# Kernel optimization log

Hardware: AMD Instinct MI355X
Metric: run time of the kernel (lower is better)

## Reference

```python
import jax, jax.numpy as jnp
import numpy as np

GN_GROUPS = 32
GN_EPS = 1e-5


def conv3x3(x, w, b=None):
    # x: [B,C,H,W], w: [O,I,3,3]
    y = jax.lax.conv_general_dilated(x, w, (1, 1), 'SAME',
                                     dimension_numbers=('NCHW', 'OIHW', 'NCHW'))
    if b is not None:
        y = y + b[None, :, None, None]
    return y


def group_norm(x, gamma, beta):
    B, C, H, W = x.shape
    xg = x.reshape(B, GN_GROUPS, C // GN_GROUPS, H, W)
    mu = xg.mean(axis=(2, 3, 4), keepdims=True)
    var = ((xg - mu) ** 2).mean(axis=(2, 3, 4), keepdims=True)
    xn = ((xg - mu) * jax.lax.rsqrt(var + GN_EPS)).reshape(B, C, H, W)
    return xn * gamma[None, :, None, None] + beta[None, :, None, None]


def tower(x, ws, gammas, betas):
    # ws: [n_conv, C, C, 3, 3]; conv(bias=False) -> GroupNorm -> ReLU, n_conv times
    for i in range(ws.shape[0]):
        x = jax.nn.relu(group_norm(conv3x3(x, ws[i]), gammas[i], betas[i]))
    return x


def setup_inputs() -> dict:
    key = jax.random.key(0)
    ks = jax.random.split(key, 20)
    C, n_conv, n_fg = 256, 4, 20  # n_class - 1 = 20
    prior = 0.01
    B = 2
    sizes = [(100, 100), (50, 50), (25, 25), (13, 13), (7, 7)]
    inp = {}
    for i, (h, w) in enumerate(sizes):
        inp[f'feat{i}'] = jax.random.normal(ks[i], (B, C, h, w), dtype=jnp.float32)
    std = 0.01  # init_conv_std
    inp['cls_tw_w'] = std * jax.random.normal(ks[5], (n_conv, C, C, 3, 3), dtype=jnp.float32)
    inp['cls_tw_g'] = jnp.ones((n_conv, C), dtype=jnp.float32)
    inp['cls_tw_b'] = jnp.zeros((n_conv, C), dtype=jnp.float32)
    inp['box_tw_w'] = std * jax.random.normal(ks[6], (n_conv, C, C, 3, 3), dtype=jnp.float32)
    inp['box_tw_g'] = jnp.ones((n_conv, C), dtype=jnp.float32)
    inp['box_tw_b'] = jnp.zeros((n_conv, C), dtype=jnp.float32)
    inp['cls_pred_w'] = std * jax.random.normal(ks[7], (n_fg, C, 3, 3), dtype=jnp.float32)
    prior_bias = -np.log((1.0 - prior) / prior)
    inp['cls_pred_b'] = jnp.full((n_fg,), prior_bias, dtype=jnp.float32)
    inp['box_pred_w'] = std * jax.random.normal(ks[8], (4, C, 3, 3), dtype=jnp.float32)
    inp['box_pred_b'] = jnp.zeros((4,), dtype=jnp.float32)
    inp['ctr_pred_w'] = std * jax.random.normal(ks[9], (1, C, 3, 3), dtype=jnp.float32)
    inp['ctr_pred_b'] = jnp.zeros((1,), dtype=jnp.float32)
    inp['scales'] = jnp.ones((5,), dtype=jnp.float32)
    return inp


def reference(feat0, feat1, feat2, feat3, feat4,
              cls_tw_w, cls_tw_g, cls_tw_b,
              box_tw_w, box_tw_g, box_tw_b,
              cls_pred_w, cls_pred_b,
              box_pred_w, box_pred_b,
              ctr_pred_w, ctr_pred_b,
              scales):
    feats = [feat0, feat1, feat2, feat3, feat4]
    logits, bboxes, centers = [], [], []
    for i, feat in enumerate(feats):
        c = tower(feat, cls_tw_w, cls_tw_g, cls_tw_b)
        logits.append(conv3x3(c, cls_pred_w, cls_pred_b))
        centers.append(conv3x3(c, ctr_pred_w, ctr_pred_b))
        b = tower(feat, box_tw_w, box_tw_g, box_tw_b)
        bboxes.append(jnp.exp(conv3x3(b, box_pred_w, box_pred_b) * scales[i]))
    return tuple(logits + bboxes + centers)
```

## Files before the change

kernel.cpp:

```cpp
#include <hip/hip_runtime.h>
#include <hip/hip_bf16.h>
#include <cstdint>

typedef unsigned short u16;
typedef __attribute__((ext_vector_type(8))) short short8;
typedef __attribute__((ext_vector_type(4))) float floatx4;
typedef __attribute__((ext_vector_type(4))) int intx4;

#define PA_TOTAL 13696
#define CCH 256
#define KTOT 2304

struct Tables {
  int H[5], W[5], P[5], base[5], tile0[5];
  int lb[5], bb[5], cb[5];
};
struct FeatPtrs { const float* f[5]; };
struct ConvArgs {
  const u16* X[2];
  const u16* Wt[2];
  u16* outB[2];
  float* stats;
  float* dout;
  const float* biasCls; const float* biasCtr; const float* biasBox; const float* scales;
};
struct ReorderArgs {
  const float* cls_w; const float* box_w; const float* pcls_w; const float* ctr_w; const float* pbox_w;
  u16* wrCls; u16* wrBox; u16* wrPCls; u16* wrPBox;
};

__device__ __forceinline__ u16 f2bf(float f) {
  union { float f; unsigned u; } v; v.f = f;
  unsigned r = v.u + 0x7fffu + ((v.u >> 16) & 1u);
  return (u16)(r >> 16);
}
__device__ __forceinline__ float bf2f(u16 h) {
  union { unsigned u; float f; } v; v.u = ((unsigned)h) << 16;
  return v.f;
}

__device__ __forceinline__ void gload16(const void* g, void* l) {
  __builtin_amdgcn_global_load_lds(
      (const __attribute__((address_space(1))) void*)g,
      (__attribute__((address_space(3))) void*)l, 16, 0, 0);
}

__global__ void reorder_all(ReorderArgs ra) {
  __shared__ float row[KTOT];
  const int r = blockIdx.x;
  const float* s;
  u16* o;
  if (r < 1024)      { s = ra.cls_w  + (size_t)r * KTOT;          o = ra.wrCls  + (size_t)r * KTOT; }
  else if (r < 2048) { int q = r - 1024; s = ra.box_w  + (size_t)q * KTOT; o = ra.wrBox  + (size_t)q * KTOT; }
  else if (r < 2068) { int q = r - 2048; s = ra.pcls_w + (size_t)q * KTOT; o = ra.wrPCls + (size_t)q * KTOT; }
  else if (r == 2068){ s = ra.ctr_w;                               o = ra.wrPCls + (size_t)20 * KTOT; }
  else if (r < 2073) { int q = r - 2069; s = ra.pbox_w + (size_t)q * KTOT; o = ra.wrPBox + (size_t)q * KTOT; }
  else if (r < 2084) {
    u16* oz = ra.wrPCls + (size_t)(21 + (r - 2073)) * KTOT;
#pragma unroll
    for (int j = 0; j < 9; ++j) oz[threadIdx.x + j * 256] = 0;
    return;
  } else {
    u16* oz = ra.wrPBox + (size_t)(4 + (r - 2084)) * KTOT;
#pragma unroll
    for (int j = 0; j < 9; ++j) oz[threadIdx.x + j * 256] = 0;
    return;
  }
#pragma unroll
  for (int j = 0; j < 9; ++j) row[threadIdx.x + j * 256] = s[threadIdx.x + j * 256];
  __syncthreads();
#pragma unroll
  for (int j = 0; j < 9; ++j) {
    int k = threadIdx.x + j * 256;
    o[k] = f2bf(row[(k & 255) * 9 + (k >> 8)]);
  }
}

__global__ void convert_inputs(FeatPtrs fp, u16* __restrict__ out, Tables tb) {
  __shared__ float tile[32][33];
  const int pt = blockIdx.x, c32 = blockIdx.y, b = blockIdx.z;
  const int p0 = pt * 32;
  int lvl = 0;
#pragma unroll
  for (int i = 1; i < 5; ++i) if (p0 >= tb.base[i]) lvl = i;
  const int P = tb.P[lvl];
  const int pl0 = p0 - tb.base[lvl];
  const int r = threadIdx.x >> 5, col = threadIdx.x & 31;
  const float* src = fp.f[lvl] + ((size_t)b * CCH + c32 * 32) * P;
#pragma unroll
  for (int i = 0; i < 4; ++i) {
    int crow = r + i * 8;
    int pl = pl0 + col;
    tile[crow][col] = (pl < P) ? src[(size_t)crow * P + pl] : 0.f;
  }
  __syncthreads();
#pragma unroll
  for (int i = 0; i < 4; ++i) {
    int px = r + i * 8;
    out[((size_t)b * PA_TOTAL + p0 + px) * CCH + c32 * 32 + col] = f2bf(tile[col][px]);
  }
}

__global__ __launch_bounds__(256) void conv_tower(ConvArgs a, Tables tb) {
  const int L = blockIdx.x + 107 * (blockIdx.y + 2 * blockIdx.z);
  const int xcd = L & 7, slot = L >> 3;
  const int tower = xcd >> 2, mt = (xcd >> 1) & 1, b = xcd & 1, t = slot;
  int lvl = 0;
#pragma unroll
  for (int i = 1; i < 5; ++i) if (t >= tb.tile0[i]) lvl = i;
  const int H = tb.H[lvl], W = tb.W[lvl], P = tb.P[lvl], base = tb.base[lvl];
  const int n0 = (t - tb.tile0[lvl]) * 128;

  const int tid = threadIdx.x;
  const int lane = tid & 63, wv = tid >> 6;
  const int wm = wv >> 1, wn = wv & 1;

  __shared__ u16 ldsAll[2 * 8192];

  const char* Xb = (const char*)(a.X[tower] + ((size_t)b * PA_TOTAL + base) * CCH);
  const char* Wb = (const char*)(a.Wt[tower] + (size_t)(mt * 128) * KTOT);

  const int qsw2 = (((lane & 3) ^ ((lane >> 2) & 3) ^ ((lane >> 4) & 3))) * 16;
  int xoffG[2];
  unsigned mask9[2];
  int xl[2];
#pragma unroll
  for (int k = 0; k < 2; ++k) {
    const int g = wv + 4 * k;
    const int prow = n0 + 16 * g + (lane >> 2);
    int rr = prow / W, cc = prow - rr * W;
    unsigned m = 0;
#pragma unroll
    for (int tap = 0; tap < 9; ++tap) {
      const int dh = tap / 3 - 1, dw = tap % 3 - 1;
      bool v = ((unsigned)(rr + dh) < (unsigned)H) & ((unsigned)(cc + dw) < (unsigned)W);
      m |= ((unsigned)v) << tap;
    }
    mask9[k] = m;
    xoffG[k] = prow * 512 + qsw2;
    xl[k] = g * 1024;
  }
  const int padbase = P * 512 + qsw2;
  int woffG[2];
#pragma unroll
  for (int k = 0; k < 2; ++k) {
    const int wrow = 16 * (wv + 4 * k) + (lane >> 2);
    woffG[k] = wrow * (KTOT * 2) + qsw2;
  }

  const int arow = lane & 15, kq = lane >> 4;
  const int csw0 = ((kq ^ (arow & 3) ^ ((arow >> 2) & 3))) * 16;
  int rbA[4], rbX[4];
#pragma unroll
  for (int i = 0; i < 4; ++i) {
    rbA[i] = (wm * 64 + i * 16 + arow) * 64 + csw0;
    rbX[i] = (wn * 64 + i * 16 + arow) * 64 + csw0;
  }

  floatx4 acc[4][4];
#pragma unroll
  for (int i = 0; i < 4; ++i)
#pragma unroll
    for (int j = 0; j < 4; ++j) acc[i][j] = (floatx4)0.f;

  {
    const int doff0 = (-W - 1) * 512;
#pragma unroll
    for (int k = 0; k < 2; ++k) {
      const int off = (mask9[k] & 1u) ? (xoffG[k] + doff0) : padbase;
      gload16(Xb + off, (char*)ldsAll + xl[k]);
    }
#pragma unroll
    for (int k = 0; k < 2; ++k)
      gload16(Wb + woffG[k], (char*)ldsAll + 8192 + xl[k]);
  }

  int pb = 0;
#pragma unroll 1
  for (int icb2 = 0; icb2 < 8; ++icb2) {
#pragma unroll
    for (int tap = 0; tap < 9; ++tap) {
      asm volatile("s_barrier" ::: "memory");
      if (!(icb2 == 7 && tap == 8)) {
        const int ntap = (tap == 8) ? 0 : tap + 1;
        const int nic  = (tap == 8) ? icb2 + 1 : icb2;
        const int ndh = ntap / 3;
        const int ndoff = ((ndh - 1) * W + (ntap - 3 * ndh - 1)) * 512;
        const int nslice = nic * 64;
        char* bufN = (char*)ldsAll + (pb ^ 1) * 16384;
#pragma unroll
        for (int k = 0; k < 2; ++k) {
          const int off = ((((mask9[k] >> ntap) & 1u) ? (xoffG[k] + ndoff) : padbase)) + nslice;
          gload16(Xb + off, bufN + xl[k]);
        }
        const int nko = ntap * 512 + nslice;
#pragma unroll
        for (int k = 0; k < 2; ++k)
          gload16(Wb + woffG[k] + nko, bufN + 8192 + xl[k]);
        asm volatile("s_waitcnt vmcnt(4)\n\ts_barrier" ::: "memory");
      } else {
        asm volatile("s_waitcnt vmcnt(0)\n\ts_barrier" ::: "memory");
      }
      const char* bufc = (const char*)ldsAll + pb * 16384;
      __builtin_amdgcn_s_setprio(1);
      short8 af[4], bv[4];
#pragma unroll
      for (int i = 0; i < 4; ++i) af[i] = *(const short8*)(bufc + 8192 + rbA[i]);
#pragma unroll
      for (int j = 0; j < 4; ++j) bv[j] = *(const short8*)(bufc + rbX[j]);
#pragma unroll
      for (int i = 0; i < 4; ++i)
#pragma unroll
        for (int j = 0; j < 4; ++j)
          acc[i][j] = __builtin_amdgcn_mfma_f32_16x16x32_bf16(af[i], bv[j], acc[i][j], 0, 0, 0);
      __builtin_amdgcn_s_setprio(0);
      pb ^= 1;
    }
  }

  const int quad = lane >> 4, col = lane & 15;
  u16* convB = a.outB[tower];
  float s[4] = {0.f, 0.f, 0.f, 0.f}, ss[4] = {0.f, 0.f, 0.f, 0.f};
#pragma unroll
  for (int j = 0; j < 4; ++j) {
    int pl = n0 + wn * 64 + j * 16 + col;
    bool valid = pl < P;
    u16* dst = convB + ((size_t)b * PA_TOTAL + base + pl) * CCH + mt * 128 + wm * 64 + quad * 4;
#pragma unroll
    for (int i = 0; i < 4; ++i) {
      ushort4 hv;
#pragma unroll
      for (int r = 0; r < 4; ++r) {
        u16 hh = f2bf(acc[i][j][r]);
        ((u16*)&hv)[r] = hh;
        float vr = bf2f(hh);
        if (valid) { s[i] += vr; ss[i] += vr * vr; }
      }
      if (valid) *(ushort4*)(dst + i * 16) = hv;
    }
  }
#pragma unroll
  for (int i = 0; i < 4; ++i) {
#pragma unroll
    for (int off = 16; off >= 1; off >>= 1) {
      s[i] += __shfl_down(s[i], off, 64);
      ss[i] += __shfl_down(ss[i], off, 64);
    }
  }
  if ((lane & 31) == 0) {
    int half = lane >> 5;
#pragma unroll
    for (int i = 0; i < 4; ++i) {
      float* st = a.stats + tower * 640 +
                  ((size_t)((b * 5 + lvl) * 32 + mt * 16 + wm * 8 + i * 2 + half)) * 2;
      atomicAdd(st, s[i]);
      atomicAdd(st + 1, ss[i]);
    }
  }
}

__global__ __launch_bounds__(256) void conv_pred(ConvArgs a, Tables tb) {
  constexpr int NI = 1;
  constexpr int WROWS = 32;
  const int L = blockIdx.x + 108 * (blockIdx.y + 2 * blockIdx.z);
  const int xcd = L & 7, slot = L >> 3;
  const int tower = xcd >> 2, b = (xcd >> 1) & 1;
  const int t = slot * 2 + (xcd & 1);
  if (t >= 107) return;
  int lvl = 0;
#pragma unroll
  for (int i = 1; i < 5; ++i) if (t >= tb.tile0[i]) lvl = i;
  const int H = tb.H[lvl], W = tb.W[lvl], P = tb.P[lvl], base = tb.base[lvl];
  const int n0 = (t - tb.tile0[lvl]) * 128;

  const int tid = threadIdx.x;
  const int lane = tid & 63, wv = tid >> 6;
  const int wm = wv >> 1, wn = wv & 1;

  __shared__ u16 ldsAll[128 * 64 + WROWS * 64];
  u16* ldsX = ldsAll;
  u16* ldsW = ldsAll + 128 * 64;

  const char* Xb = (const char*)(a.X[tower] + ((size_t)b * PA_TOTAL + base) * CCH);
  const char* Wb = (const char*)(a.Wt[tower]);

  const int qsw2 = ((lane & 7) ^ (lane >> 3)) * 16;
  int xoffG[4];
  unsigned mask9[4];
  int xlds[4];
#pragma unroll
  for (int t4 = 0; t4 < 4; ++t4) {
    int row = (t4 * 4 + wv) * 8 + (lane >> 3);
    int prow = n0 + row;
    int rr = prow / W, cc = prow - rr * W;
    unsigned m = 0;
#pragma unroll
    for (int tap = 0; tap < 9; ++tap) {
      const int dh = tap / 3 - 1, dw = tap % 3 - 1;
      bool v = ((unsigned)(rr + dh) < (unsigned)H) & ((unsigned)(cc + dw) < (unsigned)W);
      m |= ((unsigned)v) << tap;
    }
    mask9[t4] = m;
    xoffG[t4] = prow * (CCH * 2) + qsw2;
    xlds[t4] = (t4 * 4 + wv) * 1024;
  }
  const int padoff = P * (CCH * 2) + qsw2;
  int woffG[NI];
  int wlds[NI];
#pragma unroll
  for (int e = 0; e < NI; ++e) {
    int wrow = wv * 8 + (lane >> 3);
    woffG[e] = wrow * (KTOT * 2) + qsw2;
    wlds[e] = 16384 + wv * 1024;
  }

  const int arow = lane & 15, rsw = lane & 7, kq0 = lane >> 4;
  const int csw0 = (kq0 ^ rsw) * 8;
  int aoff[NI], boff[4];
#pragma unroll
  for (int i = 0; i < NI; ++i) aoff[i] = (wm * 16 + arow) * 64 + csw0;
#pragma unroll
  for (int i = 0; i < 4; ++i) boff[i] = (wn * 64 + i * 16 + arow) * 64 + csw0;

  floatx4 acc[NI][4];
#pragma unroll
  for (int i = 0; i < NI; ++i)
#pragma unroll
    for (int j = 0; j < 4; ++j) acc[i][j] = (floatx4)0.f;

#pragma unroll 1
  for (int icb = 0; icb < 4; ++icb) {
#pragma unroll
    for (int tap = 0; tap < 9; ++tap) {
      __syncthreads();
      const int ko = (tap * 256 + icb * 64) * 2;
      const int dh = tap / 3 - 1, dw = tap % 3 - 1;
      const int doff = (dh * W + dw) * (CCH * 2) + icb * 128;
#pragma unroll
      for (int t4 = 0; t4 < 4; ++t4) {
        const int off = ((mask9[t4] >> tap) & 1u) ? (xoffG[t4] + doff) : padoff;
        gload16(Xb + off, (char*)ldsAll + xlds[t4]);
      }
#pragma unroll
      for (int e = 0; e < NI; ++e)
        gload16(Wb + woffG[e] + ko, (char*)ldsAll + wlds[e]);
      asm volatile("s_waitcnt vmcnt(0) lgkmcnt(0)\n\ts_barrier" ::: "memory");
      __builtin_amdgcn_s_setprio(1);
#pragma unroll
      for (int h = 0; h < 2; ++h) {
        const int hx = h * 32;
        short8 af[NI], bv[4];
#pragma unroll
        for (int i = 0; i < NI; ++i) af[i] = *(const short8*)(ldsW + (aoff[i] ^ hx));
#pragma unroll
        for (int j = 0; j < 4; ++j) bv[j] = *(const short8*)(ldsX + (boff[j] ^ hx));
#pragma unroll
        for (int i = 0; i < NI; ++i)
#pragma unroll
          for (int j = 0; j < 4; ++j)
            acc[i][j] = __builtin_amdgcn_mfma_f32_16x16x32_bf16(af[i], bv[j], acc[i][j], 0, 0, 0);
      }
      __builtin_amdgcn_s_setprio(0);
    }
  }

  const int quad = lane >> 4, col = lane & 15;
  float* dout = a.dout;
  if (tower == 0) {
#pragma unroll
    for (int j = 0; j < 4; ++j) {
      int pl = n0 + wn * 64 + j * 16 + col;
      if (pl >= P) continue;
      int ocb = wm * 16 + quad * 4;
#pragma unroll
      for (int r = 0; r < 4; ++r) {
        int oc = ocb + r;
        float v = acc[0][j][r];
        if (oc < 20)       dout[tb.lb[lvl] + ((size_t)b * 20 + oc) * P + pl] = v + a.biasCls[oc];
        else if (oc == 20) dout[tb.cb[lvl] + (size_t)b * P + pl] = v + a.biasCtr[0];
      }
    }
  } else {
    float sc = a.scales[lvl];
#pragma unroll
    for (int j = 0; j < 4; ++j) {
      int pl = n0 + wn * 64 + j * 16 + col;
      if (pl >= P) continue;
      int ocb = wm * 16 + quad * 4;
#pragma unroll
      for (int r = 0; r < 4; ++r) {
        int oc = ocb + r;
        if (oc < 4)
          dout[tb.bb[lvl] + ((size_t)b * 4 + oc) * P + pl] = expf((acc[0][j][r] + a.biasBox[oc]) * sc);
      }
    }
  }
}

__global__ void gn_norm(const u16* __restrict__ c0, const u16* __restrict__ c1,
                        const float* __restrict__ stats,
                        const float* __restrict__ g0, const float* __restrict__ b0,
                        const float* __restrict__ g1, const float* __restrict__ b1,
                        u16* __restrict__ a0, u16* __restrict__ a1, Tables tb) {
  const int tower = blockIdx.y;
  const u16* convB = tower ? c1 : c0;
  const float* gamma = tower ? g1 : g0;
  const float* beta = tower ? b1 : b0;
  u16* act = tower ? a1 : a0;
  int idx = blockIdx.x * 256 + threadIdx.x;
  int c8 = idx & 31;
  int rest = idx >> 5;
  int p = rest % PA_TOTAL;
  int b = rest / PA_TOTAL;
  int lvl = 0;
#pragma unroll
  for (int i = 1; i < 5; ++i) if (p >= tb.base[i]) lvl = i;
  if (p - tb.base[lvl] >= tb.P[lvl]) {
    short8 z = (short8)(short)0;
    *(short8*)(act + ((size_t)b * PA_TOTAL + p) * CCH + c8 * 8) = z;
    return;
  }
  const float* st = stats + tower * 640 + ((size_t)((b * 5 + lvl) * 32 + c8)) * 2;
  float cnt = 8.f * (float)tb.P[lvl];
  float mean = st[0] / cnt;
  float var = st[1] / cnt - mean * mean;
  float inv = rsqrtf(var + 1e-5f);
  const short8 x = *(const short8*)(convB + ((size_t)b * PA_TOTAL + p) * CCH + c8 * 8);
  short8 o;
#pragma unroll
  for (int j = 0; j < 8; ++j) {
    float v = bf2f((u16)x[j]);
    float y = (v - mean) * inv * gamma[c8 * 8 + j] + beta[c8 * 8 + j];
    y = fmaxf(y, 0.f);
    o[j] = (short)f2bf(y);
  }
  *(short8*)(act + ((size_t)b * PA_TOTAL + p) * CCH + c8 * 8) = o;
}

extern "C" void kernel_launch(void* const* d_in, const int* in_sizes, int n_in,
                              void* d_out, int out_size, void* d_ws, size_t ws_size,
                              hipStream_t stream) {
  const float* feat[5];
  for (int i = 0; i < 5; ++i) feat[i] = (const float*)d_in[i];
  const float* cls_tw_w  = (const float*)d_in[5];
  const float* cls_tw_g  = (const float*)d_in[6];
  const float* cls_tw_b  = (const float*)d_in[7];
  const float* box_tw_w  = (const float*)d_in[8];
  const float* box_tw_g  = (const float*)d_in[9];
  const float* box_tw_b  = (const float*)d_in[10];
  const float* cls_pred_w = (const float*)d_in[11];
  const float* cls_pred_b = (const float*)d_in[12];
  const float* box_pred_w = (const float*)d_in[13];
  const float* box_pred_b = (const float*)d_in[14];
  const float* ctr_pred_w = (const float*)d_in[15];
  const float* ctr_pred_b = (const float*)d_in[16];
  const float* scales     = (const float*)d_in[17];
  float* out = (float*)d_out;

  char* ws = (char*)d_ws;
  float* statsAll = (float*)(ws);
  u16*   WrCls  = (u16*)(ws + 24576);
  u16*   WrBox  = (u16*)(ws + 24576 + 4718592);
  u16*   WrPCls = (u16*)(ws + 24576 + 2 * 4718592);
  u16*   WrPBox = (u16*)(ws + 24576 + 2 * 4718592 + 147456);
  u16*   bufIn   = (u16*)(ws + 10625024);
  u16*   bufAct0 = (u16*)(ws + 10625024 + 1 * (size_t)14024704);
  u16*   bufAct1 = (u16*)(ws + 10625024 + 2 * (size_t)14024704);
  u16*   bufCv0  = (u16*)(ws + 10625024 + 3 * (size_t)14024704);
  u16*   bufCv1  = (u16*)(ws + 10625024 + 4 * (size_t)14024704);

  Tables tb = { {100,50,25,13,7}, {100,50,25,13,7}, {10000,2500,625,169,49},
                {0,10112,12672,13312,13568}, {0,79,99,104,106},
                {0,400000,500000,525000,531760},
                {533720,613720,633720,638720,640072},
                {640464,660464,665464,666714,667052} };

  hipMemsetAsync(statsAll, 0, 20480, stream);

  ReorderArgs ra = { cls_tw_w, box_tw_w, cls_pred_w, ctr_pred_w, box_pred_w,
                     WrCls, WrBox, WrPCls, WrPBox };
  reorder_all<<<2112, 256, 0, stream>>>(ra);

  FeatPtrs fp = {{feat[0], feat[1], feat[2], feat[3], feat[4]}};
  convert_inputs<<<dim3(PA_TOTAL / 32, 8, 2), 256, 0, stream>>>(fp, bufIn, tb);

  ConvArgs a;
  a.dout = out;
  a.biasCls = cls_pred_b; a.biasCtr = ctr_pred_b; a.biasBox = box_pred_b; a.scales = scales;
  a.outB[0] = bufCv0; a.outB[1] = bufCv1;

  for (int s = 0; s < 4; ++s) {
    a.X[0] = (s == 0) ? bufIn : bufAct0;
    a.X[1] = (s == 0) ? bufIn : bufAct1;
    a.Wt[0] = WrCls + (size_t)s * 256 * KTOT;
    a.Wt[1] = WrBox + (size_t)s * 256 * KTOT;
    a.stats = statsAll + (size_t)s * 1280;
    conv_tower<<<dim3(107, 2, 4), 256, 0, stream>>>(a, tb);
    gn_norm<<<dim3(3424, 2), 256, 0, stream>>>(bufCv0, bufCv1, a.stats,
                                               cls_tw_g + s * 256, cls_tw_b + s * 256,
                                               box_tw_g + s * 256, box_tw_b + s * 256,
                                               bufAct0, bufAct1, tb);
  }
  a.X[0] = bufAct0; a.X[1] = bufAct1;
  a.Wt[0] = WrPCls; a.Wt[1] = WrPBox;
  conv_pred<<<dim3(108, 2, 2), 256, 0, stream>>>(a, tb);
}
```

Before: 609.4 us.

## Widen tower conv block to all 256 output channels with 64-channel K steps

Each conv_tower block now runs 512 threads (8 waves) and computes all 256 output channels for a 128-pixel tile, instead of splitting output channels across two 256-thread blocks. Each step loads a 64-channel K slice with a new 8-lane XOR swizzle. The goal is to load each activation tile once for all output channels and halve the grid. In exchange, the LDS double buffer and prefetch pipeline are removed in favour of load, wait, compute in one buffer, and the XCD-aware block mapping is dropped, so global load latency is no longer hidden behind MFMA work.

```diff
diff --git a/kernel.cpp b/kernel.cpp
--- a/kernel.cpp
+++ b/kernel.cpp
@@ -101,10 +101,8 @@
   }
 }
 
-__global__ __launch_bounds__(256) void conv_tower(ConvArgs a, Tables tb) {
-  const int L = blockIdx.x + 107 * (blockIdx.y + 2 * blockIdx.z);
-  const int xcd = L & 7, slot = L >> 3;
-  const int tower = xcd >> 2, mt = (xcd >> 1) & 1, b = xcd & 1, t = slot;
+__global__ __launch_bounds__(512) void conv_tower(ConvArgs a, Tables tb) {
+  const int t = blockIdx.x, b = blockIdx.y, tower = blockIdx.z;
   int lvl = 0;
 #pragma unroll
   for (int i = 1; i < 5; ++i) if (t >= tb.tile0[i]) lvl = i;
@@ -115,19 +113,21 @@
   const int lane = tid & 63, wv = tid >> 6;
   const int wm = wv >> 1, wn = wv & 1;
 
-  __shared__ u16 ldsAll[2 * 8192];
+  __shared__ u16 ldsAll[8192 + 16384];
+  u16* ldsX = ldsAll;
+  u16* ldsW = ldsAll + 8192;
 
   const char* Xb = (const char*)(a.X[tower] + ((size_t)b * PA_TOTAL + base) * CCH);
-  const char* Wb = (const char*)(a.Wt[tower] + (size_t)(mt * 128) * KTOT);
-
-  const int qsw2 = (((lane & 3) ^ ((lane >> 2) & 3) ^ ((lane >> 4) & 3))) * 16;
+  const char* Wb = (const char*)(a.Wt[tower]);
+
+  const int qsw2 = ((lane & 7) ^ (lane >> 3)) * 16;
   int xoffG[2];
   unsigned mask9[2];
   int xl[2];
 #pragma unroll
   for (int k = 0; k < 2; ++k) {
-    const int g = wv + 4 * k;
-    const int prow = n0 + 16 * g + (lane >> 2);
+    const int g = wv + 8 * k;
+    const int prow = n0 + 8 * g + (lane >> 3);
     int rr = prow / W, cc = prow - rr * W;
     unsigned m = 0;
 #pragma unroll
@@ -137,24 +137,26 @@
       m |= ((unsigned)v) << tap;
     }
     mask9[k] = m;
-    xoffG[k] = prow * 512 + qsw2;
+    xoffG[k] = prow * (CCH * 2) + qsw2;
     xl[k] = g * 1024;
   }
-  const int padbase = P * 512 + qsw2;
-  int woffG[2];
-#pragma unroll
-  for (int k = 0; k < 2; ++k) {
-    const int wrow = 16 * (wv + 4 * k) + (lane >> 2);
+  const int padoff = P * (CCH * 2) + qsw2;
+  int woffG[4], wl[4];
+#pragma unroll
+  for (int k = 0; k < 4; ++k) {
+    const int g = wv + 8 * k;
+    const int wrow = 8 * g + (lane >> 3);
     woffG[k] = wrow * (KTOT * 2) + qsw2;
-  }
-
-  const int arow = lane & 15, kq = lane >> 4;
-  const int csw0 = ((kq ^ (arow & 3) ^ ((arow >> 2) & 3))) * 16;
-  int rbA[4], rbX[4];
+    wl[k] = 16384 + g * 1024;
+  }
+
+  const int arow = lane & 15, rsw = lane & 7, kq0 = lane >> 4;
+  const int csw0 = (kq0 ^ rsw) * 8;
+  int aoff[4], boff[4];
 #pragma unroll
   for (int i = 0; i < 4; ++i) {
-    rbA[i] = (wm * 64 + i * 16 + arow) * 64 + csw0;
-    rbX[i] = (wn * 64 + i * 16 + arow) * 64 + csw0;
+    aoff[i] = (wm * 64 + i * 16 + arow) * 64 + csw0;
+    boff[i] = (wn * 64 + i * 16 + arow) * 64 + csw0;
   }
 
   floatx4 acc[4][4];
@@ -163,58 +165,39 @@
 #pragma unroll
     for (int j = 0; j < 4; ++j) acc[i][j] = (floatx4)0.f;
 
-  {
-    const int doff0 = (-W - 1) * 512;
-#pragma unroll
-    for (int k = 0; k < 2; ++k) {
-      const int off = (mask9[k] & 1u) ? (xoffG[k] + doff0) : padbase;
-      gload16(Xb + off, (char*)ldsAll + xl[k]);
-    }
-#pragma unroll
-    for (int k = 0; k < 2; ++k)
-      gload16(Wb + woffG[k], (char*)ldsAll + 8192 + xl[k]);
-  }
-
-  int pb = 0;
 #pragma unroll 1
-  for (int icb2 = 0; icb2 < 8; ++icb2) {
+  for (int icb = 0; icb < 4; ++icb) {
 #pragma unroll
     for (int tap = 0; tap < 9; ++tap) {
-      asm volatile("s_barrier" ::: "memory");
-      if (!(icb2 == 7 && tap == 8)) {
-        const int ntap = (tap == 8) ? 0 : tap + 1;
-        const int nic  = (tap == 8) ? icb2 + 1 : icb2;
-        const int ndh = ntap / 3;
-        const int ndoff = ((ndh - 1) * W + (ntap - 3 * ndh - 1)) * 512;
-        const int nslice = nic * 64;
-        char* bufN = (char*)ldsAll + (pb ^ 1) * 16384;
-#pragma unroll
-        for (int k = 0; k < 2; ++k) {
-          const int off = ((((mask9[k] >> ntap) & 1u) ? (xoffG[k] + ndoff) : padbase)) + nslice;
-          gload16(Xb + off, bufN + xl[k]);
-        }
-        const int nko = ntap * 512 + nslice;
-#pragma unroll
-        for (int k = 0; k < 2; ++k)
-          gload16(Wb + woffG[k] + nko, bufN + 8192 + xl[k]);
-        asm volatile("s_waitcnt vmcnt(4)\n\ts_barrier" ::: "memory");
-      } else {
-        asm volatile("s_waitcnt vmcnt(0)\n\ts_barrier" ::: "memory");
-      }
-      const char* bufc = (const char*)ldsAll + pb * 16384;
+      __syncthreads();
+      const int ko = (tap * 256 + icb * 64) * 2;
+      const int dh = tap / 3 - 1, dw = tap % 3 - 1;
+      const int doff = (dh * W + dw) * (CCH * 2) + icb * 128;
+#pragma unroll
+      for (int k = 0; k < 2; ++k) {
+        const int off = ((mask9[k] >> tap) & 1u) ? (xoffG[k] + doff) : padoff;
+        gload16(Xb + off, (char*)ldsAll + xl[k]);
+      }
+#pragma unroll
+      for (int k = 0; k < 4; ++k)
+        gload16(Wb + woffG[k] + ko, (char*)ldsAll + wl[k]);
+      asm volatile("s_waitcnt vmcnt(0) lgkmcnt(0)\n\ts_barrier" ::: "memory");
       __builtin_amdgcn_s_setprio(1);
-      short8 af[4], bv[4];
-#pragma unroll
-      for (int i = 0; i < 4; ++i) af[i] = *(const short8*)(bufc + 8192 + rbA[i]);
-#pragma unroll
-      for (int j = 0; j < 4; ++j) bv[j] = *(const short8*)(bufc + rbX[j]);
-#pragma unroll
-      for (int i = 0; i < 4; ++i)
-#pragma unroll
-        for (int j = 0; j < 4; ++j)
-          acc[i][j] = __builtin_amdgcn_mfma_f32_16x16x32_bf16(af[i], bv[j], acc[i][j], 0, 0, 0);
+#pragma unroll
+      for (int h = 0; h < 2; ++h) {
+        const int hx = h * 32;
+        short8 af[4], bv[4];
+#pragma unroll
+        for (int i = 0; i < 4; ++i) af[i] = *(const short8*)(ldsW + (aoff[i] ^ hx));
+#pragma unroll
+        for (int j = 0; j < 4; ++j) bv[j] = *(const short8*)(ldsX + (boff[j] ^ hx));
+#pragma unroll
+        for (int i = 0; i < 4; ++i)
+#pragma unroll
+          for (int j = 0; j < 4; ++j)
+            acc[i][j] = __builtin_amdgcn_mfma_f32_16x16x32_bf16(af[i], bv[j], acc[i][j], 0, 0, 0);
+      }
       __builtin_amdgcn_s_setprio(0);
-      pb ^= 1;
     }
   }
 
@@ -225,7 +208,7 @@
   for (int j = 0; j < 4; ++j) {
     int pl = n0 + wn * 64 + j * 16 + col;
     bool valid = pl < P;
-    u16* dst = convB + ((size_t)b * PA_TOTAL + base + pl) * CCH + mt * 128 + wm * 64 + quad * 4;
+    u16* dst = convB + ((size_t)b * PA_TOTAL + base + pl) * CCH + wm * 64 + quad * 4;
 #pragma unroll
     for (int i = 0; i < 4; ++i) {
       ushort4 hv;
@@ -252,7 +235,7 @@
 #pragma unroll
     for (int i = 0; i < 4; ++i) {
       float* st = a.stats + tower * 640 +
-                  ((size_t)((b * 5 + lvl) * 32 + mt * 16 + wm * 8 + i * 2 + half)) * 2;
+                  ((size_t)((b * 5 + lvl) * 32 + wm * 8 + i * 2 + half)) * 2;
       atomicAdd(st, s[i]);
       atomicAdd(st + 1, ss[i]);
     }
@@ -495,7 +478,7 @@
     a.Wt[0] = WrCls + (size_t)s * 256 * KTOT;
     a.Wt[1] = WrBox + (size_t)s * 256 * KTOT;
     a.stats = statsAll + (size_t)s * 1280;
-    conv_tower<<<dim3(107, 2, 4), 256, 0, stream>>>(a, tb);
+    conv_tower<<<dim3(107, 2, 2), 512, 0, stream>>>(a, tb);
     gn_norm<<<dim3(3424, 2), 256, 0, stream>>>(bufCv0, bufCv1, a.stats,
                                                cls_tw_g + s * 256, cls_tw_b + s * 256,
                                                box_tw_g + s * 256, box_tw_b + s * 256,
```

After: 580.2 us. 4.8% less time.
